# Optimization experiments

Hardware: AMD Instinct MI355X
Metric: run time of the kernel (lower is better)

## Reference

```python
import jax, jax.numpy as jnp
import numpy as np
from jax import lax

B, S, M, D, NQ = 128, 100, 50, 128, 10000


def _xavier(key, shape):
    fan_in, fan_out = shape[0], shape[-1]
    limit = float(np.sqrt(6.0 / (fan_in + fan_out)))
    return jax.random.uniform(key, shape, jnp.float32, -limit, limit)


def setup_inputs() -> dict:
    key = jax.random.key(0)
    ks = jax.random.split(key, 16)
    return {
        "question_seq": jax.random.randint(ks[0], (B, S), 0, NQ),
        "answer_seq": jax.random.randint(ks[1], (B, S), 0, 2),
        "emb": _xavier(ks[2], (NQ, D)),
        "key_matrix": _xavier(ks[3], (M, D)),
        "vu_w1": _xavier(ks[4], (2 * D, D)),
        "vu_b1": jnp.zeros((D,), jnp.float32),
        "vu_w2": _xavier(ks[5], (D, D)),
        "vu_b2": jnp.zeros((D,), jnp.float32),
        "er_w": _xavier(ks[6], (D, D)),
        "er_b": jnp.zeros((D,), jnp.float32),
        "ad_w": _xavier(ks[7], (D, D)),
        "ad_b": jnp.zeros((D,), jnp.float32),
        "out_w1": _xavier(ks[8], (2 * D, D)),
        "out_b1": jnp.zeros((D,), jnp.float32),
        "out_w2": _xavier(ks[9], (D, 1)),
        "out_b2": jnp.zeros((1,), jnp.float32),
    }


def reference(question_seq, answer_seq, emb, key_matrix,
              vu_w1, vu_b1, vu_w2, vu_b2,
              er_w, er_b, ad_w, ad_b,
              out_w1, out_b1, out_w2, out_b2):
    # q_embed for all steps: [B,S,D]; attention over memory slots: [B,S,M]
    q_emb = emb[question_seq]
    attn = jax.nn.softmax(jnp.einsum('bsd,md->bsm', q_emb, key_matrix), axis=-1)

    def step(v, inp):
        w, qe = inp                                   # w: [B,M], qe: [B,D]
        read = jnp.einsum('bm,bmd->bd', w, v)         # attention read
        u = jnp.concatenate([read, qe], axis=-1)      # [B,2D]
        h = jnp.tanh(u @ vu_w1 + vu_b1)
        up = h @ vu_w2 + vu_b2                        # update vector [B,D]
        e = jax.nn.sigmoid(up @ er_w + er_b)          # erase gate
        a = jnp.tanh(up @ ad_w + ad_b)                # add vector
        v = v * (1.0 - w[:, :, None] * e[:, None, :]) + w[:, :, None] * a[:, None, :]
        return v, None

    v0 = jnp.zeros((B, M, D), q_emb.dtype)
    vT, _ = lax.scan(step, v0, (attn.transpose(1, 0, 2), q_emb.transpose(1, 0, 2)))

    # predict with last question (target_question=None branch)
    last_qe = q_emb[:, -1]                            # [B,D]
    last_w = attn[:, -1]                              # [B,M]
    read = jnp.einsum('bm,bmd->bd', last_w, vT)
    p_in = jnp.concatenate([read, last_qe], axis=-1)
    h = jax.nn.relu(p_in @ out_w1 + out_b1)
    pred = jax.nn.sigmoid(h @ out_w2 + out_b2)[:, 0]  # [B]
    return pred
```

## Files before the change

### kernel.cpp

```cpp
#include <hip/hip_runtime.h>

#define BB 128
#define SS 100
#define MM 50
#define DD 128
#define KROW 66

typedef float f32x2 __attribute__((ext_vector_type(2)));

#if defined(__has_builtin)
#  if __has_builtin(__builtin_elementwise_fma)
#    define HAVE_PKFMA 1
#  endif
#  if __has_builtin(__builtin_amdgcn_update_dpp)
#    define HAVE_DPP 1
#  endif
#endif

__device__ __forceinline__ f32x2 pkfma(f32x2 a, f32x2 b, f32x2 c) {
#ifdef HAVE_PKFMA
    return __builtin_elementwise_fma(a, b, c);
#else
    f32x2 r; r.x = fmaf(a.x, b.x, c.x); r.y = fmaf(a.y, b.y, c.y); return r;
#endif
}

__device__ __forceinline__ float qbf_add(float x) {
#ifdef HAVE_DPP
    union { float f; int i; } c, o;
    c.f = x;
    o.i = __builtin_amdgcn_update_dpp(0, c.i, 0xB1, 0xF, 0xF, true);
    x += o.f;
    c.f = x;
    o.i = __builtin_amdgcn_update_dpp(0, c.i, 0x4E, 0xF, 0xF, true);
    return x + o.f;
#else
    x += __shfl_xor(x, 1);
    x += __shfl_xor(x, 2);
    return x;
#endif
}

__device__ __forceinline__ void barrier_lgkm() {
    asm volatile("s_waitcnt lgkmcnt(0)" ::: "memory");
    __builtin_amdgcn_s_barrier();
    __builtin_amdgcn_sched_barrier(0);
}

__device__ __forceinline__ float bf2f(unsigned short u) {
    union { unsigned int i; float f; } c; c.i = ((unsigned int)u) << 16; return c.f;
}
__device__ __forceinline__ float bfu_lo(unsigned int u) {
    union { unsigned int i; float f; } c; c.i = u << 16; return c.f;
}
__device__ __forceinline__ float bfu_hi(unsigned int u) {
    union { unsigned int i; float f; } c; c.i = u & 0xffff0000u; return c.f;
}
__device__ __forceinline__ unsigned short f2bf_bits(float f) {
    union { float f; unsigned int u; } c; c.f = f;
    unsigned int r = (c.u + 0x7FFFu + ((c.u >> 16) & 1u)) >> 16;
    return (unsigned short)r;
}
__device__ __forceinline__ unsigned int packbf(float lo, float hi) {
    return (unsigned int)f2bf_bits(lo) | ((unsigned int)f2bf_bits(hi) << 16);
}
__device__ __forceinline__ float fast_sigmoid(float x) { return 1.0f / (1.0f + __expf(-x)); }
__device__ __forceinline__ float fast_tanh(float x) {
    float ax = fabsf(x);
    float z = __expf(-2.0f * ax);
    float r = (1.0f - z) / (1.0f + z);
    return copysignf(r, x);
}

template <bool BF16>
__device__ __forceinline__ float ldw(const void* p, size_t idx) {
    if (BF16) return bf2f(((const unsigned short*)p)[idx]);
    return ((const float*)p)[idx];
}

__device__ __forceinline__ bool detect_bf16(const void* emb) {
    const unsigned int* eu = (const unsigned int*)emb;
    int cnt = 0;
    for (int i = 0; i < 32; ++i) {
        unsigned int e8 = (eu[i] >> 7) & 0xFFu;
        cnt += (e8 >= 100u && e8 <= 127u) ? 1 : 0;
    }
    return cnt >= 16;
}

#define W2ROW(r) ((r) * 68 + (((r) >> 5) << 3))

#define WS_WROW_OFF 0u
#define WS_QP_OFF   (BB * SS * 32u * 4u)
#define WS_W2EA_OFF (WS_QP_OFF + BB * SS * DD * 2u)
#define WS_EAB_OFF  (WS_W2EA_OFF + DD * DD * 8u)
#define WS_NEED     (WS_EAB_OFF + DD * 8u)

struct __align__(16) SmemA {
    union {
        struct {
            unsigned int key_w[MM * KROW];
            unsigned int qe8[8][68];
        } pre;
        unsigned int w2s[8724];
    } u;
};

template <bool BF16>
__device__ void pre_impl(const int* qseq, const void* emb, const void* key,
                         const void* vu_w1, unsigned int* wrow_g, unsigned short* qp_g,
                         SmemA& sm)
{
    const int t = threadIdx.x;
    const int b = blockIdx.x;
    const int half = blockIdx.y;
    const int l = t & 63;
    const int wv = t >> 6;
    const int q = l & 3;
    const int d = (wv << 4) + (l >> 2);

    if (BF16) {
        const unsigned int* kg = (const unsigned int*)key;
        for (int g = t; g < MM * 64; g += 512)
            sm.u.pre.key_w[(g >> 6) * KROW + (g & 63)] = kg[g];
    } else {
        const float* kf = (const float*)key;
        for (int g = t; g < MM * 64; g += 512) {
            int row = g >> 6, c2 = g & 63;
            sm.u.pre.key_w[row * KROW + c2] = packbf(kf[row * 128 + 2 * c2], kf[row * 128 + 2 * c2 + 1]);
        }
    }

    float rw1b[32];
#pragma unroll
    for (int i = 0; i < 32; ++i)
        rw1b[i] = ldw<BF16>(vu_w1, (size_t)(DD + 32 * q + i) * DD + d);
    __syncthreads();

    for (int ii = 0; ii < 7; ++ii) {
        const int nrows = (ii == 6) ? 2 : 8;
        {
            int r = t >> 6, w = t & 63;
            if (r < nrows) {
                int s = 50 * half + 8 * ii + r;
                int row = qseq[b * SS + s];
                if (BF16) {
                    sm.u.pre.qe8[r][w] = ((const unsigned int*)emb)[((size_t)row << 6) + w];
                } else {
                    const float* ef = (const float*)emb + (((size_t)row) << 7) + 2 * w;
                    sm.u.pre.qe8[r][w] = packbf(ef[0], ef[1]);
                }
            }
        }
        __syncthreads();

        if (wv < nrows) {
            int m = l;
            int mc = (m < MM) ? m : (MM - 1);
            float a0 = 0.f, a1 = 0.f, a2 = 0.f, a3 = 0.f;
#pragma unroll
            for (int j = 0; j < 32; ++j) {
                uint2 kw = *(const uint2*)&sm.u.pre.key_w[mc * KROW + 2 * j];
                uint2 qw = *(const uint2*)&sm.u.pre.qe8[wv][2 * j];
                a0 = fmaf(bfu_lo(kw.x), bfu_lo(qw.x), a0);
                a1 = fmaf(bfu_hi(kw.x), bfu_hi(qw.x), a1);
                a2 = fmaf(bfu_lo(kw.y), bfu_lo(qw.y), a2);
                a3 = fmaf(bfu_hi(kw.y), bfu_hi(qw.y), a3);
            }
            float lg = (a0 + a1) + (a2 + a3);
            if (m >= MM) lg = -1e30f;
            float mx = lg;
#pragma unroll
            for (int o = 32; o > 0; o >>= 1) mx = fmaxf(mx, __shfl_xor(mx, o));
            float p = (m < MM) ? __expf(lg - mx) : 0.f;
            float sum = p;
#pragma unroll
            for (int o = 32; o > 0; o >>= 1) sum += __shfl_xor(sum, o);
            p = p / sum;
            float pn = __shfl_xor(p, 4);
            int s = 50 * half + 8 * ii + wv;
            if ((m & 4) == 0)
                wrow_g[(size_t)(b * SS + s) * 32 + (m & 3) * 8 + (m >> 3)] = packbf(p, pn);
        }

        for (int sr = 0; sr < nrows; ++sr) {
            float p0 = 0.f, p1 = 0.f;
#pragma unroll
            for (int i = 0; i < 16; ++i) {
                unsigned int uw = sm.u.pre.qe8[sr][16 * q + i];
                p0 = fmaf(rw1b[2 * i],     bfu_lo(uw), p0);
                p1 = fmaf(rw1b[2 * i + 1], bfu_hi(uw), p1);
            }
            float qpv = qbf_add(p0 + p1);
            int s = 50 * half + 8 * ii + sr;
            if (q == 0) qp_g[(size_t)(b * SS + s) * DD + d] = f2bf_bits(qpv);
        }
        __syncthreads();
    }
}

template <bool BF16>
__device__ void build_impl(const void* vu_w2, const void* vu_b2,
                           const void* er_w, const void* er_b,
                           const void* ad_w, const void* ad_b,
                           f32x2* w2ea_g, f32x2* eab_g, SmemA& sm)
{
    const int t = threadIdx.x;
    const int l = t & 63;
    const int wv = t >> 6;
    const int q = l & 3;
    const int d = (wv << 4) + (l >> 2);

    if (BF16) {
        const unsigned int* wg = (const unsigned int*)vu_w2;
        for (int g = t; g < 128 * 64; g += 512)
            sm.u.w2s[W2ROW(g >> 6) + (g & 63)] = wg[g];
    } else {
        const float* wf = (const float*)vu_w2;
        for (int g = t; g < 128 * 64; g += 512) {
            int row = g >> 6, c2 = g & 63;
            sm.u.w2s[W2ROW(row) + c2] = packbf(wf[row * 128 + 2 * c2], wf[row * 128 + 2 * c2 + 1]);
        }
    }
    __syncthreads();

    f32x2 rw2ea[32];
#pragma unroll
    for (int k = 0; k < 32; ++k) { rw2ea[k].x = 0.f; rw2ea[k].y = 0.f; }
    f32x2 eab2; eab2.x = 0.f; eab2.y = 0.f;
#pragma unroll 1
    for (int jc = 0; jc < 4; ++jc) {
        f32x2 ea[32];
#pragma unroll
        for (int i = 0; i < 32; ++i) {
            int j = 32 * jc + i;
            ea[i].x = ldw<BF16>(er_w, (size_t)j * DD + d);
            ea[i].y = ldw<BF16>(ad_w, (size_t)j * DD + d);
            float b2j = ldw<BF16>(vu_b2, j);
            f32x2 bs; bs.x = b2j; bs.y = b2j;
            eab2 = pkfma(bs, ea[i], eab2);
        }
#pragma unroll
        for (int k = 0; k < 32; ++k) {
            const uint4* wp = (const uint4*)&sm.u.w2s[W2ROW(32 * q + k) + 16 * jc];
            uint4 A = wp[0], B = wp[1], C = wp[2], Dv = wp[3];
            unsigned int W[16] = { A.x, A.y, A.z, A.w, B.x, B.y, B.z, B.w,
                                   C.x, C.y, C.z, C.w, Dv.x, Dv.y, Dv.z, Dv.w };
            f32x2 acc = rw2ea[k];
#pragma unroll
            for (int wd = 0; wd < 16; ++wd) {
                float wlo = bfu_lo(W[wd]), whi = bfu_hi(W[wd]);
                f32x2 s0; s0.x = wlo; s0.y = wlo;
                f32x2 s1; s1.x = whi; s1.y = whi;
                acc = pkfma(s0, ea[2 * wd], acc);
                acc = pkfma(s1, ea[2 * wd + 1], acc);
            }
            rw2ea[k] = acc;
        }
    }
    eab2.x += ldw<BF16>(er_b, d);
    eab2.y += ldw<BF16>(ad_b, d);

#pragma unroll
    for (int k = 0; k < 32; ++k)
        w2ea_g[(size_t)(32 * q + k) * DD + d] = rw2ea[k];
    if (q == 0) eab_g[d] = eab2;
}

__global__ __launch_bounds__(512) void DKVMN_78546361909953_pre(
    const int* __restrict__ qseq,
    const void* emb, const void* key, const void* vu_w1,
    const void* vu_w2, const void* vu_b2,
    const void* er_w, const void* er_b, const void* ad_w, const void* ad_b,
    void* ws)
{
    __shared__ SmemA sm;
    unsigned int*   wrow_g = (unsigned int*)((char*)ws + WS_WROW_OFF);
    unsigned short* qp_g   = (unsigned short*)((char*)ws + WS_QP_OFF);
    f32x2*          w2ea_g = (f32x2*)((char*)ws + WS_W2EA_OFF);
    f32x2*          eab_g  = (f32x2*)((char*)ws + WS_EAB_OFF);
    bool isbf = detect_bf16(emb);
    if (blockIdx.x < BB) {
        if (isbf) pre_impl<true>(qseq, emb, key, vu_w1, wrow_g, qp_g, sm);
        else      pre_impl<false>(qseq, emb, key, vu_w1, wrow_g, qp_g, sm);
    } else if (blockIdx.y == 0) {
        if (isbf) build_impl<true>(vu_w2, vu_b2, er_w, er_b, ad_w, ad_b, w2ea_g, eab_g, sm);
        else      build_impl<false>(vu_w2, vu_b2, er_w, er_b, ad_w, ad_b, w2ea_g, eab_g, sm);
    }
}

struct __align__(16) SmemB {
    float xread[152];
    float xh[152];
    float h1f[DD];
    float qlast[DD];
};

template <bool BF16>
__device__ void scan_impl(
    const int* __restrict__ qseq,
    const void* emb, const void* vu_w1, const void* vu_b1,
    const void* out_w1, const void* out_b1, const void* out_w2, const void* out_b2,
    const unsigned int* wrow_g, const unsigned short* qp_g,
    const f32x2* w2ea_g, const f32x2* eab_g,
    void* outp, SmemB& sm)
{
    const int t = threadIdx.x;
    const int b = blockIdx.x;
    const int l = t & 63;
    const int q = l & 3;
    const int d = ((t >> 6) << 4) + (l >> 2);

    if (t < 64) {
        int row = qseq[b * SS + (SS - 1)];
        if (BF16) {
            unsigned int uw = ((const unsigned int*)emb)[((size_t)row << 6) + t];
            sm.qlast[2 * t]     = bfu_lo(uw);
            sm.qlast[2 * t + 1] = bfu_hi(uw);
        } else {
            const float* ef = (const float*)emb + (((size_t)row) << 7) + 2 * t;
            sm.qlast[2 * t]     = ef[0];
            sm.qlast[2 * t + 1] = ef[1];
        }
    }

    f32x2 rw1a2[16];
#pragma unroll
    for (int i = 0; i < 16; ++i) {
        int k0 = 32 * q + 2 * i;
        rw1a2[i].x = ldw<BF16>(vu_w1, (size_t)k0 * DD + d);
        rw1a2[i].y = ldw<BF16>(vu_w1, (size_t)(k0 + 1) * DD + d);
    }
    const float b1r = ldw<BF16>(vu_b1, d);

    f32x2 rwe2[16], rwa2[16];
#pragma unroll
    for (int i = 0; i < 16; ++i) {
        f32x2 w0 = w2ea_g[(size_t)(32 * q + 2 * i) * DD + d];
        f32x2 w1 = w2ea_g[(size_t)(32 * q + 2 * i + 1) * DD + d];
        rwe2[i].x = w0.x; rwe2[i].y = w1.x;
        rwa2[i].x = w0.y; rwa2[i].y = w1.y;
    }
    const f32x2 eab2 = eab_g[d];

    f32x2 v2[7];
#pragma unroll
    for (int p = 0; p < 7; ++p) { v2[p].x = 0.f; v2[p].y = 0.f; }
    f32x2 wr2[7];
    {
        const size_t r0 = (size_t)(b * SS) * 32 + q * 8;
        uint4 w0 = *(const uint4*)&wrow_g[r0];
        uint4 w1 = *(const uint4*)&wrow_g[r0 + 4];
        unsigned int ww[8] = { w0.x, w0.y, w0.z, w0.w, w1.x, w1.y, w1.z, w1.w };
#pragma unroll
        for (int p = 0; p < 7; ++p) { wr2[p].x = bfu_lo(ww[p]); wr2[p].y = bfu_hi(ww[p]); }
    }
    unsigned short qpcur = qp_g[(size_t)(b * SS) * DD + d];

    if (t < 152) sm.xread[t] = 0.f;
    __syncthreads();

    for (int s = 0; s < SS; ++s) {
        uint4 pwA, pwB;
        unsigned short pq = 0;
        const bool hasnext = (s + 1 < SS);
        if (hasnext) {
            size_t r1 = (size_t)(b * SS + s + 1);
            pwA = *(const uint4*)&wrow_g[r1 * 32 + q * 8];
            pwB = *(const uint4*)&wrow_g[r1 * 32 + q * 8 + 4];
            pq  = qp_g[r1 * DD + d];
        }

        {
            float hb = bf2f(qpcur) + b1r;
            const float4* xp = (const float4*)&sm.xread[40 * q];
            f32x2 accA; accA.x = 0.f; accA.y = 0.f;
            f32x2 accB; accB.x = 0.f; accB.y = 0.f;
#pragma unroll
            for (int j = 0; j < 8; ++j) {
                float4 X = xp[j];
                f32x2 x01; x01.x = X.x; x01.y = X.y;
                f32x2 x23; x23.x = X.z; x23.y = X.w;
                accA = pkfma(rw1a2[2 * j],     x01, accA);
                accB = pkfma(rw1a2[2 * j + 1], x23, accB);
            }
            float acc = qbf_add((accA.x + accB.x) + (accA.y + accB.y));
            float hh = fast_tanh(acc + hb);
            if (q == 0) sm.xh[d + 8 * (d >> 5)] = hh;
        }
        barrier_lgkm();

        {
            const float4* xp = (const float4*)&sm.xh[40 * q];
            f32x2 ae1; ae1.x = 0.f; ae1.y = 0.f;
            f32x2 ae2; ae2.x = 0.f; ae2.y = 0.f;
            f32x2 aa1; aa1.x = 0.f; aa1.y = 0.f;
            f32x2 aa2; aa2.x = 0.f; aa2.y = 0.f;
#pragma unroll
            for (int j = 0; j < 8; ++j) {
                float4 X = xp[j];
                f32x2 h01; h01.x = X.x; h01.y = X.y;
                f32x2 h23; h23.x = X.z; h23.y = X.w;
                ae1 = pkfma(rwe2[2 * j],     h01, ae1);
                aa1 = pkfma(rwa2[2 * j],     h01, aa1);
                ae2 = pkfma(rwe2[2 * j + 1], h23, ae2);
                aa2 = pkfma(rwa2[2 * j + 1], h23, aa2);
            }
            float ae = qbf_add((ae1.x + ae2.x) + (ae1.y + ae2.y));
            float aa = qbf_add((aa1.x + aa2.x) + (aa1.y + aa2.y));
            float e = fast_sigmoid(ae + eab2.x);
            float a = fast_tanh(aa + eab2.y);
            f32x2 me; me.x = -e; me.y = -e;
            f32x2 av; av.x = a;  av.y = a;
#pragma unroll
            for (int p = 0; p < 7; ++p)
                v2[p] = pkfma(wr2[p], pkfma(me, v2[p], av), v2[p]);
            if (hasnext) {
                unsigned int ww[8] = { pwA.x, pwA.y, pwA.z, pwA.w, pwB.x, pwB.y, pwB.z, pwB.w };
#pragma unroll
                for (int p = 0; p < 7; ++p) { wr2[p].x = bfu_lo(ww[p]); wr2[p].y = bfu_hi(ww[p]); }
                qpcur = pq;
            }
            f32x2 rA; rA.x = 0.f; rA.y = 0.f;
            f32x2 rB; rB.x = 0.f; rB.y = 0.f;
            rA = pkfma(wr2[0], v2[0], rA); rB = pkfma(wr2[1], v2[1], rB);
            rA = pkfma(wr2[2], v2[2], rA); rB = pkfma(wr2[3], v2[3], rB);
            rA = pkfma(wr2[4], v2[4], rA); rB = pkfma(wr2[5], v2[5], rB);
            rA = pkfma(wr2[6], v2[6], rA);
            float rr = qbf_add((rA.x + rB.x) + (rA.y + rB.y));
            if (q == 0) sm.xread[rr == rr ? (d + 8 * (d >> 5)) : 0] = rr;
        }
        barrier_lgkm();
    }

    float acc = 0.f;
    {
        const float4* xp = (const float4*)&sm.xread[40 * q];
        const float4* qp4 = (const float4*)&sm.qlast[32 * q];
#pragma unroll
        for (int j = 0; j < 8; ++j) {
            float4 xv = xp[j];
            float4 qv = qp4[j];
            int k = 32 * q + 4 * j;
            acc = fmaf(ldw<BF16>(out_w1, (size_t)k * DD + d),       xv.x, acc);
            acc = fmaf(ldw<BF16>(out_w1, (size_t)(k + 1) * DD + d), xv.y, acc);
            acc = fmaf(ldw<BF16>(out_w1, (size_t)(k + 2) * DD + d), xv.z, acc);
            acc = fmaf(ldw<BF16>(out_w1, (size_t)(k + 3) * DD + d), xv.w, acc);
            acc = fmaf(ldw<BF16>(out_w1, (size_t)(DD + k) * DD + d),     qv.x, acc);
            acc = fmaf(ldw<BF16>(out_w1, (size_t)(DD + k + 1) * DD + d), qv.y, acc);
            acc = fmaf(ldw<BF16>(out_w1, (size_t)(DD + k + 2) * DD + d), qv.z, acc);
            acc = fmaf(ldw<BF16>(out_w1, (size_t)(DD + k + 3) * DD + d), qv.w, acc);
        }
    }
    acc = qbf_add(acc);
    float h1 = fmaxf(acc + ldw<BF16>(out_b1, d), 0.f);
    if (q == 0) sm.h1f[d] = h1;
    __syncthreads();

    if (t < 64) {
        float xs = fmaf(sm.h1f[t], ldw<BF16>(out_w2, t),
                        sm.h1f[64 + t] * ldw<BF16>(out_w2, 64 + t));
#pragma unroll
        for (int o = 32; o > 0; o >>= 1) xs += __shfl_xor(xs, o);
        if (t == 0) {
            float pred = fast_sigmoid(xs + ldw<BF16>(out_b2, 0));
            if (BF16) ((unsigned short*)outp)[b] = f2bf_bits(pred);
            else      ((float*)outp)[b] = pred;
        }
    }
}

__global__ __launch_bounds__(512) void DKVMN_78546361909953_scan(
    const int* __restrict__ qseq,
    const void* emb, const void* vu_w1, const void* vu_b1,
    const void* out_w1, const void* out_b1, const void* out_w2, const void* out_b2,
    void* ws, void* outp)
{
    __shared__ SmemB sm;
    const unsigned int*   wrow_g = (const unsigned int*)((char*)ws + WS_WROW_OFF);
    const unsigned short* qp_g   = (const unsigned short*)((char*)ws + WS_QP_OFF);
    const f32x2*          w2ea_g = (const f32x2*)((char*)ws + WS_W2EA_OFF);
    const f32x2*          eab_g  = (const f32x2*)((char*)ws + WS_EAB_OFF);
    if (detect_bf16(emb))
        scan_impl<true>(qseq, emb, vu_w1, vu_b1, out_w1, out_b1, out_w2, out_b2,
                        wrow_g, qp_g, w2ea_g, eab_g, outp, sm);
    else
        scan_impl<false>(qseq, emb, vu_w1, vu_b1, out_w1, out_b1, out_w2, out_b2,
                         wrow_g, qp_g, w2ea_g, eab_g, outp, sm);
}

struct __align__(16) SmemM {
    union {
        struct {
            unsigned int key_w[MM * KROW];
            unsigned int qe8[8][68];
        } pre;
        struct {
            float xread[152];
            float xhdup[312];
            float h1f[DD];
        } run;
    } u;
    union {
        unsigned int w2s[8724];
        struct {
            unsigned int wrow_p[SS][32];
            unsigned short qp_all[SS][DD];
        } tab;
    } v2;
    int qrow[SS];
    float qlast[DD];
};

template <bool BF16>
__device__ void mono_impl(
    const int* __restrict__ qseq,
    const void* emb, const void* key,
    const void* vu_w1, const void* vu_b1, const void* vu_w2, const void* vu_b2,
    const void* er_w, const void* er_b, const void* ad_w, const void* ad_b,
    const void* out_w1, const void* out_b1, const void* out_w2, const void* out_b2,
    void* outp, SmemM& sm)
{
    const int t = threadIdx.x;
    const int b = blockIdx.x;
    const int l = t & 63;
    const int wv = t >> 6;
    const int q = l & 3;
    const int d = (wv << 4) + (l >> 2);

    if (BF16) {
        const unsigned int* kg = (const unsigned int*)key;
        for (int g = t; g < MM * 64; g += 512)
            sm.u.pre.key_w[(g >> 6) * KROW + (g & 63)] = kg[g];
        const unsigned int* wg = (const unsigned int*)vu_w2;
        for (int g = t; g < 128 * 64; g += 512)
            sm.v2.w2s[W2ROW(g >> 6) + (g & 63)] = wg[g];
    } else {
        const float* kf = (const float*)key;
        for (int g = t; g < MM * 64; g += 512) {
            int row = g >> 6, c2 = g & 63;
            sm.u.pre.key_w[row * KROW + c2] = packbf(kf[row * 128 + 2 * c2], kf[row * 128 + 2 * c2 + 1]);
        }
        const float* wf = (const float*)vu_w2;
        for (int g = t; g < 128 * 64; g += 512) {
            int row = g >> 6, c2 = g & 63;
            sm.v2.w2s[W2ROW(row) + c2] = packbf(wf[row * 128 + 2 * c2], wf[row * 128 + 2 * c2 + 1]);
        }
    }
    for (int g = t; g < SS; g += 512) sm.qrow[g] = qseq[b * SS + g];
    __syncthreads();

    f32x2 rw2ea[32];
#pragma unroll
    for (int k = 0; k < 32; ++k) { rw2ea[k].x = 0.f; rw2ea[k].y = 0.f; }
    f32x2 eab2; eab2.x = 0.f; eab2.y = 0.f;
#pragma unroll 1
    for (int jc = 0; jc < 4; ++jc) {
        f32x2 ea[32];
#pragma unroll
        for (int i = 0; i < 32; ++i) {
            int j = 32 * jc + i;
            ea[i].x = ldw<BF16>(er_w, (size_t)j * DD + d);
            ea[i].y = ldw<BF16>(ad_w, (size_t)j * DD + d);
            float b2j = ldw<BF16>(vu_b2, j);
            f32x2 bs; bs.x = b2j; bs.y = b2j;
            eab2 = pkfma(bs, ea[i], eab2);
        }
#pragma unroll
        for (int k = 0; k < 32; ++k) {
            const uint4* wp = (const uint4*)&sm.v2.w2s[W2ROW(32 * q + k) + 16 * jc];
            uint4 A = wp[0], B = wp[1], C = wp[2], Dv = wp[3];
            unsigned int W[16] = { A.x, A.y, A.z, A.w, B.x, B.y, B.z, B.w,
                                   C.x, C.y, C.z, C.w, Dv.x, Dv.y, Dv.z, Dv.w };
            f32x2 acc = rw2ea[k];
#pragma unroll
            for (int wd = 0; wd < 16; ++wd) {
                float wlo = bfu_lo(W[wd]), whi = bfu_hi(W[wd]);
                f32x2 s0; s0.x = wlo; s0.y = wlo;
                f32x2 s1; s1.x = whi; s1.y = whi;
                acc = pkfma(s0, ea[2 * wd], acc);
                acc = pkfma(s1, ea[2 * wd + 1], acc);
            }
            rw2ea[k] = acc;
        }
    }
    eab2.x += ldw<BF16>(er_b, d);
    eab2.y += ldw<BF16>(ad_b, d);
    __syncthreads();

    float rw1a[32], rw1b[32];
#pragma unroll
    for (int i = 0; i < 32; ++i) {
        rw1a[i] = ldw<BF16>(vu_w1, (size_t)(32 * q + i) * DD + d);
        rw1b[i] = ldw<BF16>(vu_w1, (size_t)(DD + 32 * q + i) * DD + d);
    }
    const float b1r = ldw<BF16>(vu_b1, d);

    for (int ii = 0; ii < 13; ++ii) {
        const int nrows = (ii == 12) ? 4 : 8;
        {
            int r = t >> 6, w = t & 63;
            if (r < nrows) {
                int row = sm.qrow[8 * ii + r];
                if (BF16) {
                    sm.u.pre.qe8[r][w] = ((const unsigned int*)emb)[((size_t)row << 6) + w];
                } else {
                    const float* ef = (const float*)emb + (((size_t)row) << 7) + 2 * w;
                    sm.u.pre.qe8[r][w] = packbf(ef[0], ef[1]);
                }
            }
        }
        __syncthreads();

        if (wv < nrows) {
            int m = l;
            int mc = (m < MM) ? m : (MM - 1);
            float a0 = 0.f, a1 = 0.f, a2 = 0.f, a3 = 0.f;
#pragma unroll
            for (int j = 0; j < 32; ++j) {
                uint2 kw = *(const uint2*)&sm.u.pre.key_w[mc * KROW + 2 * j];
                uint2 qw = *(const uint2*)&sm.u.pre.qe8[wv][2 * j];
                a0 = fmaf(bfu_lo(kw.x), bfu_lo(qw.x), a0);
                a1 = fmaf(bfu_hi(kw.x), bfu_hi(qw.x), a1);
                a2 = fmaf(bfu_lo(kw.y), bfu_lo(qw.y), a2);
                a3 = fmaf(bfu_hi(kw.y), bfu_hi(qw.y), a3);
            }
            float lg = (a0 + a1) + (a2 + a3);
            if (m >= MM) lg = -1e30f;
            float mx = lg;
#pragma unroll
            for (int o = 32; o > 0; o >>= 1) mx = fmaxf(mx, __shfl_xor(mx, o));
            float p = (m < MM) ? __expf(lg - mx) : 0.f;
            float sum = p;
#pragma unroll
            for (int o = 32; o > 0; o >>= 1) sum += __shfl_xor(sum, o);
            p = p / sum;
            float pn = __shfl_xor(p, 4);
            if ((m & 4) == 0)
                sm.v2.tab.wrow_p[8 * ii + wv][(m & 3) * 8 + (m >> 3)] = packbf(p, pn);
        }

        for (int sr = 0; sr < nrows; ++sr) {
            float p0 = 0.f, p1 = 0.f;
#pragma unroll
            for (int i = 0; i < 16; ++i) {
                unsigned int uw = sm.u.pre.qe8[sr][16 * q + i];
                p0 = fmaf(rw1b[2 * i],     bfu_lo(uw), p0);
                p1 = fmaf(rw1b[2 * i + 1], bfu_hi(uw), p1);
            }
            float qpv = qbf_add(p0 + p1);
            if (q == 0) sm.v2.tab.qp_all[8 * ii + sr][d] = f2bf_bits(qpv);
        }
        __syncthreads();
    }

    if (t < 64) {
        unsigned int uw = sm.u.pre.qe8[3][t];
        sm.qlast[2 * t]     = bfu_lo(uw);
        sm.qlast[2 * t + 1] = bfu_hi(uw);
    }
    f32x2 v2[7];
#pragma unroll
    for (int p = 0; p < 7; ++p) { v2[p].x = 0.f; v2[p].y = 0.f; }
    f32x2 wr2[7];
    {
        const uint4* wp = (const uint4*)&sm.v2.tab.wrow_p[0][q * 8];
        uint4 w0 = wp[0], w1 = wp[1];
        unsigned int ww[8] = { w0.x, w0.y, w0.z, w0.w, w1.x, w1.y, w1.z, w1.w };
#pragma unroll
        for (int p = 0; p < 7; ++p) { wr2[p].x = bfu_lo(ww[p]); wr2[p].y = bfu_hi(ww[p]); }
    }
    if (t < 152) sm.u.run.xread[t] = 0.f;
    __syncthreads();

    for (int s = 0; s < SS; ++s) {
        {
            float qpv = bf2f(sm.v2.tab.qp_all[s][d]);
            const float4* xp = (const float4*)&sm.u.run.xread[40 * q];
            f32x2 rw1a2_j;
            f32x2 acc2; acc2.x = 0.f; acc2.y = 0.f;
#pragma unroll
            for (int j = 0; j < 8; ++j) {
                float4 X = xp[j];
                f32x2 x01; x01.x = X.x; x01.y = X.y;
                f32x2 x23; x23.x = X.z; x23.y = X.w;
                rw1a2_j.x = rw1a[4 * j];     rw1a2_j.y = rw1a[4 * j + 1];
                acc2 = pkfma(rw1a2_j, x01, acc2);
                rw1a2_j.x = rw1a[4 * j + 2]; rw1a2_j.y = rw1a[4 * j + 3];
                acc2 = pkfma(rw1a2_j, x23, acc2);
            }
            float acc = qbf_add(acc2.x + acc2.y);
            float hh = fast_tanh(acc + qpv + b1r);
            if (q == 0) {
                f32x2 hd; hd.x = hh; hd.y = hh;
                *(f32x2*)&sm.u.run.xhdup[2 * d + 8 * ((2 * d) >> 5)] = hd;
            }
        }
        __syncthreads();

        {
            f32x2 acc2; acc2.x = 0.f; acc2.y = 0.f;
#pragma unroll
            for (int blk = 0; blk < 2; ++blk) {
                const float4* xp = (const float4*)&sm.u.run.xhdup[80 * q + 40 * blk];
#pragma unroll
                for (int j = 0; j < 8; ++j) {
                    float4 X = xp[j];
                    f32x2 s0; s0.x = X.x; s0.y = X.y;
                    f32x2 s1; s1.x = X.z; s1.y = X.w;
                    int k = 16 * blk + 2 * j;
                    acc2 = pkfma(rw2ea[k], s0, acc2);
                    acc2 = pkfma(rw2ea[k + 1], s1, acc2);
                }
            }
            float ae = qbf_add(acc2.x);
            float aa = qbf_add(acc2.y);
            float e = fast_sigmoid(ae + eab2.x);
            float a = fast_tanh(aa + eab2.y);
            f32x2 me; me.x = -e; me.y = -e;
            f32x2 av; av.x = a;  av.y = a;
#pragma unroll
            for (int p = 0; p < 7; ++p)
                v2[p] = pkfma(wr2[p], pkfma(me, v2[p], av), v2[p]);
            if (s + 1 < SS) {
                const uint4* wp = (const uint4*)&sm.v2.tab.wrow_p[s + 1][q * 8];
                uint4 w0 = wp[0], w1 = wp[1];
                unsigned int ww[8] = { w0.x, w0.y, w0.z, w0.w, w1.x, w1.y, w1.z, w1.w };
#pragma unroll
                for (int p = 0; p < 7; ++p) { wr2[p].x = bfu_lo(ww[p]); wr2[p].y = bfu_hi(ww[p]); }
            }
            f32x2 racc; racc.x = 0.f; racc.y = 0.f;
#pragma unroll
            for (int p = 0; p < 7; ++p)
                racc = pkfma(wr2[p], v2[p], racc);
            float rr = qbf_add(racc.x + racc.y);
            if (q == 0) sm.u.run.xread[d + 8 * (d >> 5)] = rr;
        }
        __syncthreads();
    }

    float acc = 0.f;
    {
        const float4* xp = (const float4*)&sm.u.run.xread[40 * q];
        const float4* qp4 = (const float4*)&sm.qlast[32 * q];
#pragma unroll
        for (int j = 0; j < 8; ++j) {
            float4 xv = xp[j];
            float4 qv = qp4[j];
            int k = 32 * q + 4 * j;
            acc = fmaf(ldw<BF16>(out_w1, (size_t)k * DD + d),       xv.x, acc);
            acc = fmaf(ldw<BF16>(out_w1, (size_t)(k + 1) * DD + d), xv.y, acc);
            acc = fmaf(ldw<BF16>(out_w1, (size_t)(k + 2) * DD + d), xv.z, acc);
            acc = fmaf(ldw<BF16>(out_w1, (size_t)(k + 3) * DD + d), xv.w, acc);
            acc = fmaf(ldw<BF16>(out_w1, (size_t)(DD + k) * DD + d),     qv.x, acc);
            acc = fmaf(ldw<BF16>(out_w1, (size_t)(DD + k + 1) * DD + d), qv.y, acc);
            acc = fmaf(ldw<BF16>(out_w1, (size_t)(DD + k + 2) * DD + d), qv.z, acc);
            acc = fmaf(ldw<BF16>(out_w1, (size_t)(DD + k + 3) * DD + d), qv.w, acc);
        }
    }
    acc = qbf_add(acc);
    float h1 = fmaxf(acc + ldw<BF16>(out_b1, d), 0.f);
    if (q == 0) sm.u.run.h1f[d] = h1;
    __syncthreads();

    if (t < 64) {
        float xs = fmaf(sm.u.run.h1f[t], ldw<BF16>(out_w2, t),
                        sm.u.run.h1f[64 + t] * ldw<BF16>(out_w2, 64 + t));
#pragma unroll
        for (int o = 32; o > 0; o >>= 1) xs += __shfl_xor(xs, o);
        if (t == 0) {
            float pred = fast_sigmoid(xs + ldw<BF16>(out_b2, 0));
            if (BF16) ((unsigned short*)outp)[b] = f2bf_bits(pred);
            else      ((float*)outp)[b] = pred;
        }
    }
}

__global__ __launch_bounds__(512) void DKVMN_78546361909953_kernel(
    const int* __restrict__ qseq,
    const void* emb, const void* key,
    const void* vu_w1, const void* vu_b1, const void* vu_w2, const void* vu_b2,
    const void* er_w, const void* er_b, const void* ad_w, const void* ad_b,
    const void* out_w1, const void* out_b1, const void* out_w2, const void* out_b2,
    void* outp)
{
    __shared__ SmemM sm;
    if (detect_bf16(emb))
        mono_impl<true>(qseq, emb, key, vu_w1, vu_b1, vu_w2, vu_b2,
                        er_w, er_b, ad_w, ad_b, out_w1, out_b1, out_w2, out_b2, outp, sm);
    else
        mono_impl<false>(qseq, emb, key, vu_w1, vu_b1, vu_w2, vu_b2,
                         er_w, er_b, ad_w, ad_b, out_w1, out_b1, out_w2, out_b2, outp, sm);
}

extern "C" void kernel_launch(void* const* d_in, const int* in_sizes, int n_in,
                              void* d_out, int out_size, void* d_ws, size_t ws_size,
                              hipStream_t stream) {
    const int* qseq = (const int*)d_in[0];
    if (ws_size >= (size_t)WS_NEED) {
        DKVMN_78546361909953_pre<<<dim3(BB + 1, 2), 512, 0, stream>>>(
            qseq, d_in[2], d_in[3], d_in[4],
            d_in[6], d_in[7], d_in[8], d_in[9], d_in[10], d_in[11], d_ws);
        DKVMN_78546361909953_scan<<<BB, 512, 0, stream>>>(
            qseq, d_in[2], d_in[4], d_in[5],
            d_in[12], d_in[13], d_in[14], d_in[15], d_ws, d_out);
    } else {
        DKVMN_78546361909953_kernel<<<BB, 512, 0, stream>>>(
            qseq, d_in[2], d_in[3], d_in[4], d_in[5], d_in[6], d_in[7],
            d_in[8], d_in[9], d_in[10], d_in[11],
            d_in[12], d_in[13], d_in[14], d_in[15], d_out);
    }
}
```

Measured before the change: 251.9 us.

## Stage per-batch attention and projection tables in LDS; use fast reciprocal

Before the sequential scan starts, the scan kernel copies each batch's full attention-weight rows and precomputed qe projections from global memory into shared memory, so the per-step prefetches become LDS reads rather than global loads on the serial critical path. Divisions in sigmoid, tanh and softmax normalisation are replaced with the hardware reciprocal builtin. The dot-product accumulations are split across more independent packed accumulators to shorten dependency chains. In exchange, shared memory use grows by about 38 KB per block, which may reduce occupancy, and the reciprocal is slightly less precise than a true division.

```diff
diff --git a/kernel.cpp b/kernel.cpp
--- a/kernel.cpp
+++ b/kernel.cpp
@@ -14,6 +14,9 @@
 #  endif
 #  if __has_builtin(__builtin_amdgcn_update_dpp)
 #    define HAVE_DPP 1
+#  endif
+#  if __has_builtin(__builtin_amdgcn_rcpf)
+#    define HAVE_RCP 1
 #  endif
 #endif
 
@@ -64,11 +67,20 @@
 __device__ __forceinline__ unsigned int packbf(float lo, float hi) {
     return (unsigned int)f2bf_bits(lo) | ((unsigned int)f2bf_bits(hi) << 16);
 }
-__device__ __forceinline__ float fast_sigmoid(float x) { return 1.0f / (1.0f + __expf(-x)); }
+__device__ __forceinline__ float fast_rcp(float x) {
+#ifdef HAVE_RCP
+    return __builtin_amdgcn_rcpf(x);
+#else
+    return 1.0f / x;
+#endif
+}
+__device__ __forceinline__ float fast_sigmoid(float x) {
+    return fast_rcp(1.0f + __expf(-x));
+}
 __device__ __forceinline__ float fast_tanh(float x) {
     float ax = fabsf(x);
     float z = __expf(-2.0f * ax);
-    float r = (1.0f - z) / (1.0f + z);
+    float r = (1.0f - z) * fast_rcp(1.0f + z);
     return copysignf(r, x);
 }
 
@@ -176,7 +188,7 @@
             float sum = p;
 #pragma unroll
             for (int o = 32; o > 0; o >>= 1) sum += __shfl_xor(sum, o);
-            p = p / sum;
+            p = p * fast_rcp(sum);
             float pn = __shfl_xor(p, 4);
             int s = 50 * half + 8 * ii + wv;
             if ((m & 4) == 0)
@@ -294,6 +306,8 @@
     float xh[152];
     float h1f[DD];
     float qlast[DD];
+    unsigned int   wtab[SS][32];
+    unsigned short qptab[SS][DD];
 };
 
 template <bool BF16>
@@ -311,6 +325,15 @@
     const int q = l & 3;
     const int d = ((t >> 6) << 4) + (l >> 2);
 
+    {
+        const uint4* srcw = (const uint4*)(wrow_g + (size_t)b * SS * 32);
+        uint4* dstw = (uint4*)&sm.wtab[0][0];
+        for (int g = t; g < SS * 32 / 4; g += 512) dstw[g] = srcw[g];
+        const uint4* srcq = (const uint4*)(qp_g + (size_t)b * SS * DD);
+        uint4* dstq = (uint4*)&sm.qptab[0][0];
+        for (int g = t; g < SS * DD / 8; g += 512) dstq[g] = srcq[g];
+    }
+
     if (t < 64) {
         int row = qseq[b * SS + (SS - 1)];
         if (BF16) {
@@ -346,45 +369,51 @@
     f32x2 v2[7];
 #pragma unroll
     for (int p = 0; p < 7; ++p) { v2[p].x = 0.f; v2[p].y = 0.f; }
+
+    if (t < 152) sm.xread[t] = 0.f;
+    __syncthreads();
+
     f32x2 wr2[7];
     {
-        const size_t r0 = (size_t)(b * SS) * 32 + q * 8;
-        uint4 w0 = *(const uint4*)&wrow_g[r0];
-        uint4 w1 = *(const uint4*)&wrow_g[r0 + 4];
+        uint4 w0 = *(const uint4*)&sm.wtab[0][q * 8];
+        uint4 w1 = *(const uint4*)&sm.wtab[0][q * 8 + 4];
         unsigned int ww[8] = { w0.x, w0.y, w0.z, w0.w, w1.x, w1.y, w1.z, w1.w };
 #pragma unroll
         for (int p = 0; p < 7; ++p) { wr2[p].x = bfu_lo(ww[p]); wr2[p].y = bfu_hi(ww[p]); }
     }
-    unsigned short qpcur = qp_g[(size_t)(b * SS) * DD + d];
-
-    if (t < 152) sm.xread[t] = 0.f;
-    __syncthreads();
+    unsigned short qpcur = sm.qptab[0][d];
 
     for (int s = 0; s < SS; ++s) {
         uint4 pwA, pwB;
         unsigned short pq = 0;
         const bool hasnext = (s + 1 < SS);
         if (hasnext) {
-            size_t r1 = (size_t)(b * SS + s + 1);
-            pwA = *(const uint4*)&wrow_g[r1 * 32 + q * 8];
-            pwB = *(const uint4*)&wrow_g[r1 * 32 + q * 8 + 4];
-            pq  = qp_g[r1 * DD + d];
+            pwA = *(const uint4*)&sm.wtab[s + 1][q * 8];
+            pwB = *(const uint4*)&sm.wtab[s + 1][q * 8 + 4];
+            pq  = sm.qptab[s + 1][d];
         }
 
         {
             float hb = bf2f(qpcur) + b1r;
             const float4* xp = (const float4*)&sm.xread[40 * q];
-            f32x2 accA; accA.x = 0.f; accA.y = 0.f;
-            f32x2 accB; accB.x = 0.f; accB.y = 0.f;
-#pragma unroll
-            for (int j = 0; j < 8; ++j) {
-                float4 X = xp[j];
+            f32x2 acc0, acc1, acc2, acc3;
+            acc0.x = 0.f; acc0.y = 0.f; acc1.x = 0.f; acc1.y = 0.f;
+            acc2.x = 0.f; acc2.y = 0.f; acc3.x = 0.f; acc3.y = 0.f;
+#pragma unroll
+            for (int j = 0; j < 4; ++j) {
+                float4 X = xp[2 * j];
+                float4 Y = xp[2 * j + 1];
                 f32x2 x01; x01.x = X.x; x01.y = X.y;
                 f32x2 x23; x23.x = X.z; x23.y = X.w;
-                accA = pkfma(rw1a2[2 * j],     x01, accA);
-                accB = pkfma(rw1a2[2 * j + 1], x23, accB);
-            }
-            float acc = qbf_add((accA.x + accB.x) + (accA.y + accB.y));
+                f32x2 y01; y01.x = Y.x; y01.y = Y.y;
+                f32x2 y23; y23.x = Y.z; y23.y = Y.w;
+                acc0 = pkfma(rw1a2[4 * j],     x01, acc0);
+                acc1 = pkfma(rw1a2[4 * j + 1], x23, acc1);
+                acc2 = pkfma(rw1a2[4 * j + 2], y01, acc2);
+                acc3 = pkfma(rw1a2[4 * j + 3], y23, acc3);
+            }
+            f32x2 ap = (acc0 + acc1) + (acc2 + acc3);
+            float acc = qbf_add(ap.x + ap.y);
             float hh = fast_tanh(acc + hb);
             if (q == 0) sm.xh[d + 8 * (d >> 5)] = hh;
         }
@@ -392,22 +421,32 @@
 
         {
             const float4* xp = (const float4*)&sm.xh[40 * q];
-            f32x2 ae1; ae1.x = 0.f; ae1.y = 0.f;
-            f32x2 ae2; ae2.x = 0.f; ae2.y = 0.f;
-            f32x2 aa1; aa1.x = 0.f; aa1.y = 0.f;
-            f32x2 aa2; aa2.x = 0.f; aa2.y = 0.f;
-#pragma unroll
-            for (int j = 0; j < 8; ++j) {
-                float4 X = xp[j];
+            f32x2 ae0, ae1, ae2, ae3, aa0, aa1, aa2, aa3;
+            ae0.x = 0.f; ae0.y = 0.f; ae1.x = 0.f; ae1.y = 0.f;
+            ae2.x = 0.f; ae2.y = 0.f; ae3.x = 0.f; ae3.y = 0.f;
+            aa0.x = 0.f; aa0.y = 0.f; aa1.x = 0.f; aa1.y = 0.f;
+            aa2.x = 0.f; aa2.y = 0.f; aa3.x = 0.f; aa3.y = 0.f;
+#pragma unroll
+            for (int j = 0; j < 4; ++j) {
+                float4 X = xp[2 * j];
+                float4 Y = xp[2 * j + 1];
                 f32x2 h01; h01.x = X.x; h01.y = X.y;
                 f32x2 h23; h23.x = X.z; h23.y = X.w;
-                ae1 = pkfma(rwe2[2 * j],     h01, ae1);
-                aa1 = pkfma(rwa2[2 * j],     h01, aa1);
-                ae2 = pkfma(rwe2[2 * j + 1], h23, ae2);
-                aa2 = pkfma(rwa2[2 * j + 1], h23, aa2);
-            }
-            float ae = qbf_add((ae1.x + ae2.x) + (ae1.y + ae2.y));
-            float aa = qbf_add((aa1.x + aa2.x) + (aa1.y + aa2.y));
+                f32x2 h45; h45.x = Y.x; h45.y = Y.y;
+                f32x2 h67; h67.x = Y.z; h67.y = Y.w;
+                ae0 = pkfma(rwe2[4 * j],     h01, ae0);
+                aa0 = pkfma(rwa2[4 * j],     h01, aa0);
+                ae1 = pkfma(rwe2[4 * j + 1], h23, ae1);
+                aa1 = pkfma(rwa2[4 * j + 1], h23, aa1);
+                ae2 = pkfma(rwe2[4 * j + 2], h45, ae2);
+                aa2 = pkfma(rwa2[4 * j + 2], h45, aa2);
+                ae3 = pkfma(rwe2[4 * j + 3], h67, ae3);
+                aa3 = pkfma(rwa2[4 * j + 3], h67, aa3);
+            }
+            f32x2 aep = (ae0 + ae1) + (ae2 + ae3);
+            f32x2 aap = (aa0 + aa1) + (aa2 + aa3);
+            float ae = qbf_add(aep.x + aep.y);
+            float aa = qbf_add(aap.x + aap.y);
             float e = fast_sigmoid(ae + eab2.x);
             float a = fast_tanh(aa + eab2.y);
             f32x2 me; me.x = -e; me.y = -e;
@@ -634,7 +673,7 @@
             float sum = p;
 #pragma unroll
             for (int o = 32; o > 0; o >>= 1) sum += __shfl_xor(sum, o);
-            p = p / sum;
+            p = p * fast_rcp(sum);
             float pn = __shfl_xor(p, 4);
             if ((m & 4) == 0)
                 sm.v2.tab.wrow_p[8 * ii + wv][(m & 3) * 8 + (m >> 3)] = packbf(p, pn);
```

New measurement: 247.0 us. About the same (-1.9%).
